# Kernel tuning notes

Hardware: AMD Instinct MI355X
Metric: run time of the kernel (lower is better)

The kernel has to match this reference:

```python
import jax, jax.numpy as jnp
import numpy as np


def setup_inputs() -> dict:
    key = jax.random.key(0)
    ks = jax.random.split(key, 6)
    B, C, H, W = 8, 256, 32, 32
    d = C // 8  # 32
    return {
        "x": jax.random.normal(ks[0], (B, C, H, W), dtype=jnp.float32),
        "Wq": jax.random.normal(ks[1], (d, C), dtype=jnp.float32) * 0.05,
        "bq": jnp.zeros((d,), dtype=jnp.float32),
        "Wk": jax.random.normal(ks[2], (d, C), dtype=jnp.float32) * 0.05,
        "bk": jnp.zeros((d,), dtype=jnp.float32),
        "Wv": jax.random.normal(ks[3], (C, C), dtype=jnp.float32) * 0.05,
        "bv": jnp.zeros((C,), dtype=jnp.float32),
        "Wr": jax.random.normal(ks[4], (d, 2), dtype=jnp.float32) * 0.05,
        "br": jnp.zeros((d,), dtype=jnp.float32),
        "gamma": jnp.array([0.5], dtype=jnp.float32),
    }


def reference(x, Wq, bq, Wk, bk, Wv, bv, Wr, br, gamma):
    B, C, H, W = x.shape
    N = H * W
    d = Wq.shape[0]
    xf = x.reshape(B, C, N)

    # 1x1 convs == per-pixel linear projections
    q = jnp.einsum('dc,bcn->bdn', Wq, xf) + bq[None, :, None]  # (B,d,N)
    k = jnp.einsum('dc,bcn->bdn', Wk, xf) + bk[None, :, None]  # (B,d,N)
    v = jnp.einsum('oc,bcn->bon', Wv, xf) + bv[None, :, None]  # (B,C,N)

    # relative position code: pairwise coord diffs through 1x1 conv (batch-independent)
    gh, gw = jnp.meshgrid(jnp.linspace(0.0, 1.0, H), jnp.linspace(0.0, 1.0, W), indexing='ij')
    coords = jnp.stack([gh.reshape(-1), gw.reshape(-1)])  # (2,N)
    diff = coords[:, :, None] - coords[:, None, :]         # (2,N,N)
    rp_code = jnp.einsum('dt,tij->dij', Wr, diff) + br[:, None, None]  # (d,N,N)

    scale = 1.0 / jnp.sqrt(jnp.asarray(d, dtype=x.dtype))
    score = jnp.einsum('bdi,bdj->bij', q, k) * scale          # (B,N,N)
    rp_score = jnp.einsum('bdi,dij->bij', q, rp_code) * scale  # (B,N,N)
    attn = jax.nn.softmax(score + rp_score, axis=-1)

    # out[b,c,i] = sum_j v[b,c,j] * attn[b,i,j]
    out = jnp.einsum('bcj,bij->bci', v, attn)
    return gamma[0] * out.reshape(B, C, H, W) + x
```

## Files before the change

### kernel.cpp

```cpp
#include <hip/hip_runtime.h>
#include <hip/hip_bf16.h>

#define BATCH 8
#define CH    256
#define NN    1024
#define DD    32

#define QT_OFF 0
#define KT_OFF (BATCH * NN * DD)
#define V_OFF  (2 * BATCH * NN * DD)
#define V2_B   (NN * CH)
#define WF_OFF (V_OFF + BATCH * V2_B)

#define SCALE_Q (0.17677669529663687f * 1.4426950408889634f)
#define INV31 (1.0f / 31.0f)

typedef __attribute__((ext_vector_type(4))) float f32x4;
typedef __attribute__((ext_vector_type(8))) short bf16x8;

__device__ __forceinline__ unsigned int packbf2(float lo, float hi) {
    __hip_bfloat162 h = __float22bfloat162_rn(make_float2(lo, hi));
    union { __hip_bfloat162 h; unsigned int u; } cv; cv.h = h;
    return cv.u;
}
__device__ __forceinline__ unsigned short f2bf(float x) {
    union { float f; unsigned int u; } v; v.f = x;
    return (unsigned short)((v.u + 0x7FFFu + ((v.u >> 16) & 1u)) >> 16);
}

__global__ __launch_bounds__(256) void wrepack_kernel(
    const float* __restrict__ Wq, const float* __restrict__ Wk,
    const float* __restrict__ Wv, unsigned short* __restrict__ ws)
{
    const int gid = blockIdx.x * 256 + threadIdx.x;
    const int e = gid * 4;
    const int m = e >> 8;
    const int k = e & 255;
    const float* src = (m < 32) ? (Wq + m * CH + k)
                     : (m < 64) ? (Wk + (m - 32) * CH + k)
                                : (Wv + (m - 64) * CH + k);
    const float4 w = *(const float4*)src;
    const int mf = m >> 4, kc = k >> 5;
    const int lf = ((k >> 3) & 3) * 16 + (m & 15);
    const int jj = k & 7;
    uint2 st = { packbf2(w.x, w.y), packbf2(w.z, w.w) };
    *(uint2*)(ws + WF_OFF + ((size_t)(mf * 8 + kc) * 64 + lf) * 8 + jj) = st;
}

__global__ __launch_bounds__(256, 2) void proj_kernel(
    const float* __restrict__ x,
    const float* __restrict__ bq, const float* __restrict__ bk,
    const float* __restrict__ bv, const float* __restrict__ Wr,
    unsigned short* __restrict__ ws)
{
    const int nt   = blockIdx.x;
    const int b    = blockIdx.y;
    const int tid  = threadIdx.x;
    const int wv   = tid >> 6;
    const int lane = tid & 63;
    const int n16  = lane & 15;
    const int q4   = lane >> 4;
    const int n    = nt * 16 + n16;

    f32x4 acc[5];
#pragma unroll
    for (int t = 0; t < 5; t++) acc[t] = (f32x4){0.f, 0.f, 0.f, 0.f};

    const unsigned short* wfl = ws + WF_OFF + (size_t)lane * 8;
    const float* xb = x + (size_t)b * CH * NN + n;

    float  bx[2][8];
    bf16x8 af[2][5];
#pragma unroll
    for (int jj = 0; jj < 8; jj++)
        bx[0][jj] = xb[(size_t)(q4 * 8 + jj) * NN];
#pragma unroll
    for (int t = 0; t < 5; t++)
        af[0][t] = *(const bf16x8*)(wfl + (size_t)((wv * 5 + t) * 8) * 512);

#pragma unroll
    for (int kc = 0; kc < 8; kc++) {
        const int s = kc & 1;
        if (kc < 7) {
            const int kofs = (kc + 1) * 32 + q4 * 8;
#pragma unroll
            for (int jj = 0; jj < 8; jj++)
                bx[s ^ 1][jj] = xb[(size_t)(kofs + jj) * NN];
#pragma unroll
            for (int t = 0; t < 5; t++)
                af[s ^ 1][t] = *(const bf16x8*)(wfl + (size_t)((wv * 5 + t) * 8 + kc + 1) * 512);
        }
        union { unsigned int u[4]; bf16x8 v; } bf;
#pragma unroll
        for (int p = 0; p < 4; p++) bf.u[p] = packbf2(bx[s][2 * p], bx[s][2 * p + 1]);
#pragma unroll
        for (int t = 0; t < 5; t++)
            acc[t] = __builtin_amdgcn_mfma_f32_16x16x32_bf16(af[s][t], bf.v, acc[t], 0, 0, 0);
    }

    const int jt  = n >> 5;
    const int q4p = (n >> 3) & 3;
    const int jj  = n & 7;
#pragma unroll
    for (int t = 0; t < 5; t++) {
        const int mf = wv * 5 + t;
        const int mb = mf * 16 + q4 * 4;
        if (mb < 32) {
            const float r0 = (acc[t][0] + bq[mb + 0]) * SCALE_Q;
            const float r1 = (acc[t][1] + bq[mb + 1]) * SCALE_Q;
            const float r2 = (acc[t][2] + bq[mb + 2]) * SCALE_Q;
            const float r3 = (acc[t][3] + bq[mb + 3]) * SCALE_Q;
            uint2 st = { packbf2(r0, r1), packbf2(r2, r3) };
            *(uint2*)(ws + QT_OFF + (size_t)(b * NN + n) * DD + mb) = st;
        } else if (mb < 64) {
            const int d = mb - 32;
            const float An = (float)(n >> 5) * INV31;
            const float Bn = (float)(n & 31) * INV31;
            float r[4];
#pragma unroll
            for (int rr = 0; rr < 4; rr++)
                r[rr] = acc[t][rr] + bk[d + rr] - An * Wr[2 * (d + rr)] - Bn * Wr[2 * (d + rr) + 1];
            uint2 st = { packbf2(r[0], r[1]), packbf2(r[2], r[3]) };
            *(uint2*)(ws + KT_OFF + (size_t)(b * NN + n) * DD + d) = st;
        } else {
            const int c = mb - 64;
#pragma unroll
            for (int rr = 0; rr < 4; rr++) {
                const int cc = c + rr;
                const size_t off = V_OFF + (size_t)b * V2_B
                                 + (size_t)jt * 8192 + (size_t)(cc >> 4) * 512
                                 + (size_t)(q4p * 16 + (cc & 15)) * 8 + jj;
                ws[off] = f2bf(acc[t][rr] + bv[cc]);
            }
        }
    }
}

__global__ __launch_bounds__(256, 4) void attn_kernel(
    const float* __restrict__ x,
    const float* __restrict__ gamma,
    const unsigned short* __restrict__ ws,
    float* __restrict__ out)
{
    const int b    = blockIdx.x;
    const int by   = blockIdx.y;
    const int ig   = by >> 1;
    const int cs   = by & 1;
    const int tid  = threadIdx.x;
    const int jh   = tid >> 7;
    const int cw   = (tid >> 6) & 1;
    const int lane = tid & 63;
    const int n    = lane & 15;
    const int q4   = lane >> 4;
    const int i0   = ig * 16;
    const int cb   = cs * 128 + cw * 64;

    __shared__ float accL[2 * 16 * 64];
    __shared__ float lL[16];

    const unsigned short* qT = ws + QT_OFF + (size_t)b * NN * DD;
    const unsigned short* kT = ws + KT_OFF + (size_t)b * NN * DD + (size_t)jh * 512 * DD;
    const unsigned short* vb = ws + V_OFF + (size_t)b * V2_B
                             + (size_t)jh * 16 * 8192 + (size_t)(cb >> 4) * 512
                             + (size_t)lane * 8;

    const bf16x8 qf = *(const bf16x8*)(qT + (size_t)(i0 + n) * DD + q4 * 8);

    f32x4 acc[4];
#pragma unroll
    for (int t = 0; t < 4; t++) acc[t] = (f32x4){0.f, 0.f, 0.f, 0.f};
    float lsum = 0.f;

    bf16x8 ka0 = *(const bf16x8*)(kT + (size_t)(n) * DD + q4 * 8);
    bf16x8 ka1 = *(const bf16x8*)(kT + (size_t)(16 + n) * DD + q4 * 8);
    bf16x8 va[4];
#pragma unroll
    for (int t = 0; t < 4; t++)
        va[t] = *(const bf16x8*)(vb + t * 512);

    const int qh2 = (q4 & 1) * 2;
    int src[4];
#pragma unroll
    for (int t = 0; t < 4; t++) src[t] = (qh2 + (t >> 1)) * 16 + n;

#pragma unroll 4
    for (int ch = 0; ch < 16; ch++) {
        const bf16x8 ka0c = ka0, ka1c = ka1;
        bf16x8 vac[4];
#pragma unroll
        for (int t = 0; t < 4; t++) vac[t] = va[t];

        {
            const int j0 = (ch + 1) * 32;
            ka0 = *(const bf16x8*)(kT + (size_t)(j0 + n) * DD + q4 * 8);
            ka1 = *(const bf16x8*)(kT + (size_t)(j0 + 16 + n) * DD + q4 * 8);
#pragma unroll
            for (int t = 0; t < 4; t++)
                va[t] = *(const bf16x8*)(vb + (ch + 1) * 8192 + t * 512);
        }

        const f32x4 z = {0.f, 0.f, 0.f, 0.f};
        f32x4 s0 = __builtin_amdgcn_mfma_f32_16x16x32_bf16(ka0c, qf, z, 0, 0, 0);
        f32x4 s1 = __builtin_amdgcn_mfma_f32_16x16x32_bf16(ka1c, qf, z, 0, 0, 0);

        float p0[4], p1[4];
#pragma unroll
        for (int r = 0; r < 4; r++) {
            p0[r] = exp2f(s0[r]);
            p1[r] = exp2f(s1[r]);
            lsum += p0[r] + p1[r];
        }

        unsigned int pk0[2] = { packbf2(p0[0], p0[1]), packbf2(p0[2], p0[3]) };
        unsigned int pk1[2] = { packbf2(p1[0], p1[1]), packbf2(p1[2], p1[3]) };
        union { unsigned int u[4]; bf16x8 v; } pf;
#pragma unroll
        for (int t = 0; t < 4; t++) {
            const unsigned int lo = (unsigned int)__shfl((int)pk0[t & 1], src[t], 64);
            const unsigned int hi = (unsigned int)__shfl((int)pk1[t & 1], src[t], 64);
            pf.u[t] = (q4 >= 2) ? hi : lo;
        }

#pragma unroll
        for (int t = 0; t < 4; t++)
            acc[t] = __builtin_amdgcn_mfma_f32_16x16x32_bf16(vac[t], pf.v, acc[t], 0, 0, 0);
    }

    lsum += __shfl_xor(lsum, 16, 64);
    lsum += __shfl_xor(lsum, 32, 64);

    if (jh == 1) {
#pragma unroll
        for (int t = 0; t < 4; t++)
#pragma unroll
            for (int r = 0; r < 4; r++)
                accL[(cw * 16 + t * 4 + r) * 64 + lane] = acc[t][r];
        if (cw == 0 && lane < 16) lL[lane] = lsum;
    }
    __syncthreads();

    if (jh == 0) {
        const float rl = gamma[0] / (lsum + lL[n]);
#pragma unroll
        for (int t = 0; t < 4; t++) {
#pragma unroll
            for (int r = 0; r < 4; r++) {
                const int c = cb + t * 16 + q4 * 4 + r;
                const size_t idx = (size_t)(b * CH + c) * NN + i0 + n;
                const float a = acc[t][r] + accL[(cw * 16 + t * 4 + r) * 64 + lane];
                out[idx] = a * rl + x[idx];
            }
        }
    }
}

extern "C" void kernel_launch(void* const* d_in, const int* in_sizes, int n_in,
                              void* d_out, int out_size, void* d_ws, size_t ws_size,
                              hipStream_t stream) {
    (void)in_sizes; (void)n_in; (void)out_size; (void)ws_size;
    const float* x     = (const float*)d_in[0];
    const float* Wq    = (const float*)d_in[1];
    const float* bq    = (const float*)d_in[2];
    const float* Wk    = (const float*)d_in[3];
    const float* bk    = (const float*)d_in[4];
    const float* Wv    = (const float*)d_in[5];
    const float* bv    = (const float*)d_in[6];
    const float* Wr    = (const float*)d_in[7];
    const float* gamma = (const float*)d_in[9];
    float* out = (float*)d_out;
    unsigned short* ws = (unsigned short*)d_ws;

    wrepack_kernel<<<80, 256, 0, stream>>>(Wq, Wk, Wv, ws);
    proj_kernel<<<dim3(64, 8), 256, 0, stream>>>(x, bq, bk, bv, Wr, ws);
    attn_kernel<<<dim3(8, 128), 256, 0, stream>>>(x, gamma, ws, out);
}
```

Baseline: 108.0 us.

## Retile attention blocks to 32 query rows by 64 channels

Each block now handles two 16-row query tiles and a quarter of the channels instead of one query tile and half the channels. Every wave reuses its K and V fragments across both query tiles, which halves V fragment loads per output. In exchange, each wave computes twice as many score MFMAs and exponentials per channel column, so redundant softmax work across channel-splitting waves doubles. The grid shape is unchanged.

```diff
diff --git a/kernel.cpp b/kernel.cpp
--- a/kernel.cpp
+++ b/kernel.cpp
@@ -144,19 +144,19 @@
 {
     const int b    = blockIdx.x;
     const int by   = blockIdx.y;
-    const int ig   = by >> 1;
-    const int cs   = by & 1;
+    const int ig   = by >> 2;
+    const int cq   = by & 3;
     const int tid  = threadIdx.x;
     const int jh   = tid >> 7;
     const int cw   = (tid >> 6) & 1;
     const int lane = tid & 63;
     const int n    = lane & 15;
     const int q4   = lane >> 4;
-    const int i0   = ig * 16;
-    const int cb   = cs * 128 + cw * 64;
+    const int i0   = ig * 32;
+    const int cb   = cq * 64 + cw * 32;
 
     __shared__ float accL[2 * 16 * 64];
-    __shared__ float lL[16];
+    __shared__ float lL[32];
 
     const unsigned short* qT = ws + QT_OFF + (size_t)b * NN * DD;
     const unsigned short* kT = ws + KT_OFF + (size_t)b * NN * DD + (size_t)jh * 512 * DD;
@@ -164,18 +164,22 @@
                              + (size_t)jh * 16 * 8192 + (size_t)(cb >> 4) * 512
                              + (size_t)lane * 8;
 
-    const bf16x8 qf = *(const bf16x8*)(qT + (size_t)(i0 + n) * DD + q4 * 8);
-
-    f32x4 acc[4];
-#pragma unroll
-    for (int t = 0; t < 4; t++) acc[t] = (f32x4){0.f, 0.f, 0.f, 0.f};
-    float lsum = 0.f;
+    const bf16x8 qf0 = *(const bf16x8*)(qT + (size_t)(i0 + n) * DD + q4 * 8);
+    const bf16x8 qf1 = *(const bf16x8*)(qT + (size_t)(i0 + 16 + n) * DD + q4 * 8);
+
+    f32x4 acc0[2], acc1[2];
+#pragma unroll
+    for (int t = 0; t < 2; t++) {
+        acc0[t] = (f32x4){0.f, 0.f, 0.f, 0.f};
+        acc1[t] = (f32x4){0.f, 0.f, 0.f, 0.f};
+    }
+    float lsum0 = 0.f, lsum1 = 0.f;
 
     bf16x8 ka0 = *(const bf16x8*)(kT + (size_t)(n) * DD + q4 * 8);
     bf16x8 ka1 = *(const bf16x8*)(kT + (size_t)(16 + n) * DD + q4 * 8);
-    bf16x8 va[4];
-#pragma unroll
-    for (int t = 0; t < 4; t++)
+    bf16x8 va[2];
+#pragma unroll
+    for (int t = 0; t < 2; t++)
         va[t] = *(const bf16x8*)(vb + t * 512);
 
     const int qh2 = (q4 & 1) * 2;
@@ -186,69 +190,90 @@
 #pragma unroll 4
     for (int ch = 0; ch < 16; ch++) {
         const bf16x8 ka0c = ka0, ka1c = ka1;
-        bf16x8 vac[4];
-#pragma unroll
-        for (int t = 0; t < 4; t++) vac[t] = va[t];
+        bf16x8 vac[2];
+#pragma unroll
+        for (int t = 0; t < 2; t++) vac[t] = va[t];
 
         {
             const int j0 = (ch + 1) * 32;
             ka0 = *(const bf16x8*)(kT + (size_t)(j0 + n) * DD + q4 * 8);
             ka1 = *(const bf16x8*)(kT + (size_t)(j0 + 16 + n) * DD + q4 * 8);
 #pragma unroll
-            for (int t = 0; t < 4; t++)
+            for (int t = 0; t < 2; t++)
                 va[t] = *(const bf16x8*)(vb + (ch + 1) * 8192 + t * 512);
         }
 
         const f32x4 z = {0.f, 0.f, 0.f, 0.f};
-        f32x4 s0 = __builtin_amdgcn_mfma_f32_16x16x32_bf16(ka0c, qf, z, 0, 0, 0);
-        f32x4 s1 = __builtin_amdgcn_mfma_f32_16x16x32_bf16(ka1c, qf, z, 0, 0, 0);
-
-        float p0[4], p1[4];
+        f32x4 s0a = __builtin_amdgcn_mfma_f32_16x16x32_bf16(ka0c, qf0, z, 0, 0, 0);
+        f32x4 s1a = __builtin_amdgcn_mfma_f32_16x16x32_bf16(ka1c, qf0, z, 0, 0, 0);
+        f32x4 s0b = __builtin_amdgcn_mfma_f32_16x16x32_bf16(ka0c, qf1, z, 0, 0, 0);
+        f32x4 s1b = __builtin_amdgcn_mfma_f32_16x16x32_bf16(ka1c, qf1, z, 0, 0, 0);
+
+        float p0a[4], p1a[4], p0b[4], p1b[4];
 #pragma unroll
         for (int r = 0; r < 4; r++) {
-            p0[r] = exp2f(s0[r]);
-            p1[r] = exp2f(s1[r]);
-            lsum += p0[r] + p1[r];
-        }
-
-        unsigned int pk0[2] = { packbf2(p0[0], p0[1]), packbf2(p0[2], p0[3]) };
-        unsigned int pk1[2] = { packbf2(p1[0], p1[1]), packbf2(p1[2], p1[3]) };
-        union { unsigned int u[4]; bf16x8 v; } pf;
+            p0a[r] = exp2f(s0a[r]);
+            p1a[r] = exp2f(s1a[r]);
+            p0b[r] = exp2f(s0b[r]);
+            p1b[r] = exp2f(s1b[r]);
+            lsum0 += p0a[r] + p1a[r];
+            lsum1 += p0b[r] + p1b[r];
+        }
+
+        unsigned int pk0a[2] = { packbf2(p0a[0], p0a[1]), packbf2(p0a[2], p0a[3]) };
+        unsigned int pk1a[2] = { packbf2(p1a[0], p1a[1]), packbf2(p1a[2], p1a[3]) };
+        unsigned int pk0b[2] = { packbf2(p0b[0], p0b[1]), packbf2(p0b[2], p0b[3]) };
+        unsigned int pk1b[2] = { packbf2(p1b[0], p1b[1]), packbf2(p1b[2], p1b[3]) };
+        union { unsigned int u[4]; bf16x8 v; } pfa, pfb;
 #pragma unroll
         for (int t = 0; t < 4; t++) {
-            const unsigned int lo = (unsigned int)__shfl((int)pk0[t & 1], src[t], 64);
-            const unsigned int hi = (unsigned int)__shfl((int)pk1[t & 1], src[t], 64);
-            pf.u[t] = (q4 >= 2) ? hi : lo;
-        }
-
-#pragma unroll
-        for (int t = 0; t < 4; t++)
-            acc[t] = __builtin_amdgcn_mfma_f32_16x16x32_bf16(vac[t], pf.v, acc[t], 0, 0, 0);
-    }
-
-    lsum += __shfl_xor(lsum, 16, 64);
-    lsum += __shfl_xor(lsum, 32, 64);
+            const unsigned int loa = (unsigned int)__shfl((int)pk0a[t & 1], src[t], 64);
+            const unsigned int hia = (unsigned int)__shfl((int)pk1a[t & 1], src[t], 64);
+            const unsigned int lob = (unsigned int)__shfl((int)pk0b[t & 1], src[t], 64);
+            const unsigned int hib = (unsigned int)__shfl((int)pk1b[t & 1], src[t], 64);
+            pfa.u[t] = (q4 >= 2) ? hia : loa;
+            pfb.u[t] = (q4 >= 2) ? hib : lob;
+        }
+
+#pragma unroll
+        for (int t = 0; t < 2; t++) {
+            acc0[t] = __builtin_amdgcn_mfma_f32_16x16x32_bf16(vac[t], pfa.v, acc0[t], 0, 0, 0);
+            acc1[t] = __builtin_amdgcn_mfma_f32_16x16x32_bf16(vac[t], pfb.v, acc1[t], 0, 0, 0);
+        }
+    }
+
+    lsum0 += __shfl_xor(lsum0, 16, 64);
+    lsum0 += __shfl_xor(lsum0, 32, 64);
+    lsum1 += __shfl_xor(lsum1, 16, 64);
+    lsum1 += __shfl_xor(lsum1, 32, 64);
 
     if (jh == 1) {
 #pragma unroll
-        for (int t = 0; t < 4; t++)
-#pragma unroll
-            for (int r = 0; r < 4; r++)
-                accL[(cw * 16 + t * 4 + r) * 64 + lane] = acc[t][r];
-        if (cw == 0 && lane < 16) lL[lane] = lsum;
+        for (int t = 0; t < 2; t++)
+#pragma unroll
+            for (int r = 0; r < 4; r++) {
+                accL[(cw * 16 + t * 4 + r) * 64 + lane]     = acc0[t][r];
+                accL[(cw * 16 + 8 + t * 4 + r) * 64 + lane] = acc1[t][r];
+            }
+        if (cw == 0 && lane < 16) lL[lane] = lsum0;
+        if (cw == 1 && lane < 16) lL[16 + lane] = lsum1;
     }
     __syncthreads();
 
     if (jh == 0) {
-        const float rl = gamma[0] / (lsum + lL[n]);
-#pragma unroll
-        for (int t = 0; t < 4; t++) {
+        const float g = gamma[0];
+        const float rl0 = g / (lsum0 + lL[n]);
+        const float rl1 = g / (lsum1 + lL[16 + n]);
+#pragma unroll
+        for (int t = 0; t < 2; t++) {
 #pragma unroll
             for (int r = 0; r < 4; r++) {
                 const int c = cb + t * 16 + q4 * 4 + r;
-                const size_t idx = (size_t)(b * CH + c) * NN + i0 + n;
-                const float a = acc[t][r] + accL[(cw * 16 + t * 4 + r) * 64 + lane];
-                out[idx] = a * rl + x[idx];
+                const size_t base = (size_t)(b * CH + c) * NN + i0 + n;
+                const float a0 = acc0[t][r] + accL[(cw * 16 + t * 4 + r) * 64 + lane];
+                const float a1 = acc1[t][r] + accL[(cw * 16 + 8 + t * 4 + r) * 64 + lane];
+                out[base]      = a0 * rl0 + x[base];
+                out[base + 16] = a1 * rl1 + x[base + 16];
             }
         }
     }
```

After: 116.4 us. +7.7%, slower.
